# Kernel optimization log

Hardware: AMD Instinct MI355X
Metric: run time of the kernel (lower is better)

## Reference

```python
import jax, jax.numpy as jnp
import numpy as np

B, L, DW, DP = 128, 512, 256, 64
NF = 512          # num_filters == types == nr (forced by U.view / maxpool in source)
D = DW + 2 * DP   # 384
DWIN = 3 * D      # windowed feature width


def setup_inputs() -> dict:
    key = jax.random.key(0)
    ks = jax.random.split(key, 10)
    return {
        "x": jax.random.normal(ks[0], (B, L, DW), jnp.float32),
        "e1": jax.random.normal(ks[1], (B, DW), jnp.float32),
        "e2": jax.random.normal(ks[2], (B, DW), jnp.float32),
        "posVec": jax.random.normal(ks[3], (B, L, 2 * DP), jnp.float32),
        "We1": jax.random.normal(ks[4], (DW, DW), jnp.float32),
        "We2": jax.random.normal(ks[5], (DW, DW), jnp.float32),
        "U": jax.random.normal(ks[6], (NF, NF), jnp.float32),
        "conv_w": jax.random.normal(ks[7], (NF, DWIN), jnp.float32) * 0.02,
        "conv_b": jnp.zeros((NF,), jnp.float32),
        "rel_w": jax.random.normal(ks[8], (NF, NF), jnp.float32) * 0.02,  # y_embedding.weight (nr, num_filters)
    }


def reference(x, e1, e2, posVec, We1, We2, U, conv_w, conv_b, rel_w):
    # ---- input attention ----
    x_concat = jnp.concatenate([x, posVec], axis=-1)            # (B, L, D)
    px = jnp.pad(x_concat, ((0, 0), (1, 1), (0, 0)))            # pad seq by k=1
    w_concat = jnp.concatenate(
        [px[:, 0:L], px[:, 1:L + 1], px[:, 2:L + 2]], axis=-1)  # (B, L, 3D)
    A1 = jnp.einsum('bld,de,be->bl', x, We1, e1)                # (B, L)
    A2 = jnp.einsum('bld,de,be->bl', x, We2, e2)
    alpha = 0.5 * (jax.nn.softmax(A1, axis=1) + jax.nn.softmax(A2, axis=1))
    R = w_concat * alpha[:, :, None]                            # (B, L, 3D)
    # ---- convolution (kernel spans full window -> per-position linear) ----
    conv = jnp.tanh(jnp.einsum('bld,fd->bfl', R, conv_w) + conv_b[None, :, None])  # (B, F, L)
    # ---- attentive pooling ----
    G = jnp.einsum('bfl,ft,rt->blr', conv, U, rel_w)            # (B, L, nr)
    AP = jax.nn.softmax(G, axis=1)                              # softmax over seq positions
    wo = jnp.einsum('bfl,blr->bfr', conv, AP)                   # (B, F, nr)
    wo = jnp.max(wo, axis=2)                                    # MaxPool2d((1, types)) -> (B, F)
    wo = jax.nn.relu(wo)
    return wo, rel_w
```

## Files before the change

kernel.cpp:

```cpp
#include <hip/hip_runtime.h>
#include <hip/hip_bf16.h>

#define BB 128
#define LL 512
#define DW 256
#define DP 64
#define NF 512
#define DD 384
#define DWIN 1152
#define RR 512
#define LP 514

typedef __attribute__((ext_vector_type(8))) short short8;
typedef __attribute__((ext_vector_type(4))) short short4v;
typedef __attribute__((ext_vector_type(2))) short short2v;
typedef __attribute__((ext_vector_type(8))) _Float16 half8;
typedef __attribute__((ext_vector_type(4))) float f32x4;
typedef __attribute__((ext_vector_type(2))) float f32x2;

typedef __attribute__((address_space(1))) const void* gas_t;
typedef __attribute__((address_space(3))) void* las_t;

__device__ __forceinline__ void stage16(const void* g, void* l) {
    __builtin_amdgcn_global_load_lds((gas_t)g, (las_t)l, 16, 0, 0);
}

__device__ inline short f2h(float v) {
    _Float16 h = (_Float16)v;
    return *reinterpret_cast<short*>(&h);
}
__device__ inline int xcd_swz(int bid, int nwg) {
    return (bid & 7) * (nwg >> 3) + (bid >> 3);
}

__global__ void k_ve(const float* __restrict__ We1, const float* __restrict__ We2,
                     const float* __restrict__ e1, const float* __restrict__ e2,
                     float* __restrict__ v1, float* __restrict__ v2) {
    int b = blockIdx.x;
    int d = threadIdx.x;
    __shared__ float s1[DW], s2[DW];
    s1[d] = e1[b * DW + d];
    s2[d] = e2[b * DW + d];
    __syncthreads();
    float a1 = 0.f, a2 = 0.f;
    for (int e = 0; e < DW; ++e) {
        a1 += We1[d * DW + e] * s1[e];
        a2 += We2[d * DW + e] * s2[e];
    }
    v1[b * DW + d] = a1;
    v2[b * DW + d] = a2;
}

__global__ __launch_bounds__(256) void k_pack_logits(
    const float* __restrict__ x, const float* __restrict__ pv,
    const float* __restrict__ v1, const float* __restrict__ v2,
    short* __restrict__ pxp, float* __restrict__ A1, float* __restrict__ A2) {
    int gr = blockIdx.x * 4 + (threadIdx.x >> 6);
    int lane = threadIdx.x & 63;
    int b = gr / LP;
    int rr = gr - b * LP;
    short* dst = pxp + (size_t)gr * DD;
    if (rr == 0 || rr == LP - 1) {
        *(short4v*)(dst + lane * 4) = (short4v){0, 0, 0, 0};
        *(short2v*)(dst + 256 + lane * 2) = (short2v){0, 0};
        return;
    }
    int l = rr - 1;
    f32x4 xv = *(const f32x4*)(x + ((size_t)b * LL + l) * DW + lane * 4);
    f32x2 pvv = *(const f32x2*)(pv + ((size_t)b * LL + l) * (2 * DP) + lane * 2);
    f32x4 w1 = *(const f32x4*)(v1 + b * DW + lane * 4);
    f32x4 w2 = *(const f32x4*)(v2 + b * DW + lane * 4);
    float p1 = xv[0] * w1[0] + xv[1] * w1[1] + xv[2] * w1[2] + xv[3] * w1[3];
    float p2 = xv[0] * w2[0] + xv[1] * w2[1] + xv[2] * w2[2] + xv[3] * w2[3];
    for (int off = 32; off; off >>= 1) {
        p1 += __shfl_down(p1, off);
        p2 += __shfl_down(p2, off);
    }
    short4v ox;
#pragma unroll
    for (int j = 0; j < 4; ++j) ox[j] = f2h(xv[j]);
    *(short4v*)(dst + lane * 4) = ox;
    short2v op;
    op[0] = f2h(pvv[0]);
    op[1] = f2h(pvv[1]);
    *(short2v*)(dst + 256 + lane * 2) = op;
    if (lane == 0) { A1[b * LL + l] = p1; A2[b * LL + l] = p2; }
}

__global__ void k_alpha(const float* __restrict__ A1, const float* __restrict__ A2,
                        float* __restrict__ alpha) {
    int b = blockIdx.x;
    int l = threadIdx.x;
    __shared__ float s[LL];
    float a1 = A1[b * LL + l], a2 = A2[b * LL + l];

    s[l] = a1; __syncthreads();
    for (int st = 256; st; st >>= 1) { if (l < st) s[l] = fmaxf(s[l], s[l + st]); __syncthreads(); }
    float m1 = s[0]; __syncthreads();
    float e1x = expf(a1 - m1);
    s[l] = e1x; __syncthreads();
    for (int st = 256; st; st >>= 1) { if (l < st) s[l] += s[l + st]; __syncthreads(); }
    float d1 = s[0]; __syncthreads();

    s[l] = a2; __syncthreads();
    for (int st = 256; st; st >>= 1) { if (l < st) s[l] = fmaxf(s[l], s[l + st]); __syncthreads(); }
    float m2 = s[0]; __syncthreads();
    float e2x = expf(a2 - m2);
    s[l] = e2x; __syncthreads();
    for (int st = 256; st; st >>= 1) { if (l < st) s[l] += s[l + st]; __syncthreads(); }
    float d2 = s[0];

    alpha[b * LL + l] = 0.5f * (e1x / d1 + e2x / d2);
}

__global__ __launch_bounds__(256) void k_pack_w(const float* __restrict__ cw,
                                                short* __restrict__ cwb) {
    int idx = blockIdx.x * 256 + threadIdx.x;
    const float* src = cw + (size_t)idx * 8;
    f32x4 u0 = *(const f32x4*)(src);
    f32x4 u1 = *(const f32x4*)(src + 4);
    short8 v;
#pragma unroll
    for (int jj = 0; jj < 4; ++jj) { v[jj] = f2h(u0[jj]); v[jj + 4] = f2h(u1[jj]); }
    *(short8*)(cwb + (size_t)idx * 8) = v;
}

__global__ void k_w2t(const float* __restrict__ U, const float* __restrict__ relw,
                      short* __restrict__ Qf) {
    __shared__ float As[16][65], Bs[16][65];
    int r0 = blockIdx.y * 64, f0 = blockIdx.x * 64;
    int tid = threadIdx.x, ty = tid >> 4, tx = tid & 15;
    float acc[4][4] = {};
    for (int k0 = 0; k0 < NF; k0 += 16) {
        for (int i = 0; i < 4; ++i) {
            int lin = tid + 256 * i;
            int kk = lin & 15, mm = lin >> 4;
            As[kk][mm] = relw[(r0 + mm) * NF + k0 + kk];
            Bs[kk][mm] = U[(f0 + mm) * NF + k0 + kk];
        }
        __syncthreads();
        for (int kk = 0; kk < 16; ++kk) {
            float av[4], bv[4];
            for (int i = 0; i < 4; ++i) av[i] = As[kk][ty * 4 + i];
            for (int j = 0; j < 4; ++j) bv[j] = Bs[kk][tx * 4 + j];
            for (int i = 0; i < 4; ++i)
                for (int j = 0; j < 4; ++j) acc[i][j] += av[i] * bv[j];
        }
        __syncthreads();
    }
    for (int i = 0; i < 4; ++i)
        for (int j = 0; j < 4; ++j)
            Qf[(size_t)(r0 + ty * 4 + i) * NF + f0 + tx * 4 + j] = f2h(acc[i][j]);
}

__global__ __launch_bounds__(256) void k_conv_mfma(
    const short* __restrict__ pxp, const short* __restrict__ cwb,
    const float* __restrict__ conv_b, const float* __restrict__ alpha,
    short* __restrict__ conv_lf, short* __restrict__ conv_fl) {
    int wg = xcd_swz(blockIdx.x, 2048);
    int b = wg >> 4;
    int l0 = ((wg >> 2) & 3) * 128;
    int f0 = (wg & 3) * 128;
    int tid = threadIdx.x;
    int lane = tid & 63, w = tid >> 6;
    int wm = w >> 1, wn = w & 1;
    int lr = lane & 15, lg = lane >> 4;

    __shared__ __align__(16) char smem[34816];
    short (*As)[32] = (short(*)[32])smem;
    short (*Bs)[32] = (short(*)[32])(smem + 8192);
    short (*T)[136] = (short(*)[136])smem;

    f32x4 acc[4][4];
    for (int i = 0; i < 4; ++i)
        for (int j = 0; j < 4; ++j) acc[i][j] = (f32x4){0.f, 0.f, 0.f, 0.f};

    int rowA = lane >> 2;
    int sw = (lane & 3) ^ ((rowA >> 1) & 3);
    const short* gA = pxp + ((size_t)b * LP + l0 + w * 32 + rowA) * DD + sw * 8;
    const short* gB = cwb + (size_t)(f0 + w * 32 + rowA) * DWIN + sw * 8;
    short* lA = &As[w * 32][0];
    short* lB = &Bs[w * 32][0];
    int rsw = (lg ^ ((lr >> 1) & 3)) * 8;
    int rA = wm * 64, rB = wn * 64;

    for (int kb = 0; kb < 36; ++kb) {
        int k0 = kb * 32;
        stage16(gA + k0, lA);
        stage16(gA + 16 * DD + k0, lA + 16 * 32);
        stage16(gB + k0, lB);
        stage16(gB + (size_t)16 * DWIN + k0, lB + 16 * 32);
        __syncthreads();
        half8 af[4], bf[4];
#pragma unroll
        for (int mi = 0; mi < 4; ++mi)
            af[mi] = *(const half8*)(&As[rA + mi * 16 + lr][rsw]);
#pragma unroll
        for (int ni = 0; ni < 4; ++ni)
            bf[ni] = *(const half8*)(&Bs[rB + ni * 16 + lr][rsw]);
#pragma unroll
        for (int mi = 0; mi < 4; ++mi)
#pragma unroll
            for (int ni = 0; ni < 4; ++ni)
                acc[mi][ni] = __builtin_amdgcn_mfma_f32_16x16x32_f16(
                    af[mi], bf[ni], acc[mi][ni], 0, 0, 0);
        __syncthreads();
    }

    int lbase = l0 + wm * 64, fbase = f0 + wn * 64;
#pragma unroll
    for (int mi = 0; mi < 4; ++mi) {
        f32x4 av = *(const f32x4*)(alpha + (size_t)b * LL + lbase + mi * 16 + lg * 4);
        int lrow = lbase + mi * 16 + lg * 4;
#pragma unroll
        for (int ni = 0; ni < 4; ++ni) {
            int f = fbase + ni * 16 + lr;
            float bias = conv_b[f];
            short4v o;
#pragma unroll
            for (int r = 0; r < 4; ++r) {
                float val = tanhf(av[r] * acc[mi][ni][r] + bias);
                short sv = f2h(val);
                o[r] = sv;
                conv_lf[((size_t)b * LL + lrow + r) * NF + f] = sv;
            }
            *(short4v*)(&T[wn * 64 + ni * 16 + lr][wm * 64 + mi * 16 + lg * 4]) = o;
        }
    }
    __syncthreads();
#pragma unroll
    for (int i = 0; i < 8; ++i) {
        int lin = tid + 256 * i;
        int frow = lin >> 4;
        int q = lin & 15;
        short8 v = *(const short8*)(&T[frow][q * 8]);
        *(short8*)(conv_fl + ((size_t)b * NF + f0 + frow) * LL + l0 + q * 8) = v;
    }
}


__global__ __launch_bounds__(256) void k_g_mfma(
    const short* __restrict__ Qf,
    const short* __restrict__ convlf, _Float16* __restrict__ Gp) {
    int wg = xcd_swz(blockIdx.x, 2048);
    int b = wg >> 4;
    int r0 = ((wg >> 2) & 3) * 128;
    int l0 = (wg & 3) * 128;
    int tid = threadIdx.x, lane = tid & 63, w = tid >> 6;
    int wm = w >> 1, wn = w & 1;
    int lr = lane & 15, lg = lane >> 4;

    __shared__ __align__(16) short As[128][64];
    __shared__ __align__(16) short Bs[128][64];

    f32x4 acc[4][4];
    for (int i = 0; i < 4; ++i)
        for (int j = 0; j < 4; ++j) acc[i][j] = (f32x4){0.f, 0.f, 0.f, 0.f};

    int rowA = lane >> 3;
    int sw = (lane & 7) ^ rowA;
    const short* gA = Qf + (size_t)(r0 + w * 32 + rowA) * NF + sw * 8;
    const short* gB = convlf + (size_t)b * LL * NF + (size_t)(l0 + w * 32 + rowA) * NF + sw * 8;
    short* lA = &As[w * 32][0];
    short* lB = &Bs[w * 32][0];
    int rA = wm * 64, rB = wn * 64;
    int p7 = lr & 7;

    for (int kb = 0; kb < 8; ++kb) {
        int k0 = kb * 64;
#pragma unroll
        for (int c = 0; c < 4; ++c) {
            stage16(gA + (size_t)(8 * c) * NF + k0, lA + c * 8 * 64);
            stage16(gB + (size_t)(8 * c) * NF + k0, lB + c * 8 * 64);
        }
        __syncthreads();
#pragma unroll
        for (int kk = 0; kk < 2; ++kk) {
            half8 af[4], bf[4];
            int cs = ((kk << 2) + lg);
#pragma unroll
            for (int mi = 0; mi < 4; ++mi)
                af[mi] = *(const half8*)(&As[rA + mi * 16 + lr][(cs ^ p7) * 8]);
#pragma unroll
            for (int ni = 0; ni < 4; ++ni)
                bf[ni] = *(const half8*)(&Bs[rB + ni * 16 + lr][(cs ^ p7) * 8]);
#pragma unroll
            for (int mi = 0; mi < 4; ++mi)
#pragma unroll
                for (int ni = 0; ni < 4; ++ni)
                    acc[mi][ni] = __builtin_amdgcn_mfma_f32_16x16x32_f16(
                        af[mi], bf[ni], acc[mi][ni], 0, 0, 0);
        }
        __syncthreads();
    }

    int rbase = r0 + wm * 64, lbase = l0 + wn * 64;
#pragma unroll
    for (int mi = 0; mi < 4; ++mi)
#pragma unroll
        for (int ni = 0; ni < 4; ++ni)
#pragma unroll
            for (int rr = 0; rr < 4; ++rr) {
                int r = rbase + mi * 16 + lg * 4 + rr;
                int l = lbase + ni * 16 + lr;
                Gp[((size_t)b * RR + r) * LL + l] = (_Float16)acc[mi][ni][rr];
            }
}

__global__ __launch_bounds__(256) void k_softmax(_Float16* __restrict__ Gp) {
    const float LOG2E = 1.4426950408889634f;
    int row = blockIdx.x * 4 + (threadIdx.x >> 6);
    int lane = threadIdx.x & 63;
    _Float16* base = Gp + (size_t)row * LL;
    half8 hv = *(const half8*)(base + lane * 8);
    float v[8];
#pragma unroll
    for (int j = 0; j < 8; ++j) v[j] = (float)hv[j];
    float m = v[0];
#pragma unroll
    for (int j = 1; j < 8; ++j) m = fmaxf(m, v[j]);
    for (int off = 1; off < 64; off <<= 1) m = fmaxf(m, __shfl_xor(m, off));
    float s = 0.f;
    float p[8];
#pragma unroll
    for (int j = 0; j < 8; ++j) { p[j] = exp2f((v[j] - m) * LOG2E); s += p[j]; }
    for (int off = 1; off < 64; off <<= 1) s += __shfl_xor(s, off);
    float inv = 1.f / s;
    short8 o;
#pragma unroll
    for (int j = 0; j < 8; ++j) o[j] = f2h(p[j] * inv);
    *(short8*)((short*)base + lane * 8) = o;
}

__global__ __launch_bounds__(256) void k_wo_mfma(
    const short* __restrict__ convfl, const short* __restrict__ P,
    float* __restrict__ out) {
    int wg = xcd_swz(blockIdx.x, 2048);
    int b = wg >> 4;
    int f0 = ((wg >> 2) & 3) * 128;
    int r0 = (wg & 3) * 128;
    int tid = threadIdx.x, lane = tid & 63, w = tid >> 6;
    int wm = w >> 1, wn = w & 1;
    int lr = lane & 15, lg = lane >> 4;

    __shared__ __align__(16) short As[128][64];
    __shared__ __align__(16) short Bs[128][64];

    f32x4 acc[4][4];
    for (int i = 0; i < 4; ++i)
        for (int j = 0; j < 4; ++j) acc[i][j] = (f32x4){0.f, 0.f, 0.f, 0.f};

    int rowA = lane >> 3;
    int sw = (lane & 7) ^ rowA;
    const short* gA = convfl + (size_t)b * NF * LL + (size_t)(f0 + w * 32 + rowA) * LL + sw * 8;
    const short* gB = P + (size_t)b * RR * LL + (size_t)(r0 + w * 32 + rowA) * LL + sw * 8;
    short* lA = &As[w * 32][0];
    short* lB = &Bs[w * 32][0];
    int rA = wm * 64, rB = wn * 64;
    int p7 = lr & 7;

    for (int kb = 0; kb < 8; ++kb) {
        int k0 = kb * 64;
#pragma unroll
        for (int c = 0; c < 4; ++c) {
            stage16(gA + (size_t)(8 * c) * LL + k0, lA + c * 8 * 64);
            stage16(gB + (size_t)(8 * c) * LL + k0, lB + c * 8 * 64);
        }
        __syncthreads();
#pragma unroll
        for (int kk = 0; kk < 2; ++kk) {
            half8 af[4], bf[4];
            int cs = ((kk << 2) + lg);
#pragma unroll
            for (int mi = 0; mi < 4; ++mi)
                af[mi] = *(const half8*)(&As[rA + mi * 16 + lr][(cs ^ p7) * 8]);
#pragma unroll
            for (int ni = 0; ni < 4; ++ni)
                bf[ni] = *(const half8*)(&Bs[rB + ni * 16 + lr][(cs ^ p7) * 8]);
#pragma unroll
            for (int mi = 0; mi < 4; ++mi)
#pragma unroll
                for (int ni = 0; ni < 4; ++ni)
                    acc[mi][ni] = __builtin_amdgcn_mfma_f32_16x16x32_f16(
                        af[mi], bf[ni], acc[mi][ni], 0, 0, 0);
        }
        __syncthreads();
    }

    int fbase = f0 + wm * 64;
#pragma unroll
    for (int mi = 0; mi < 4; ++mi)
#pragma unroll
        for (int rr = 0; rr < 4; ++rr) {
            float m = acc[mi][0][rr];
#pragma unroll
            for (int ni = 1; ni < 4; ++ni) m = fmaxf(m, acc[mi][ni][rr]);
            m = fmaxf(m, __shfl_xor(m, 1));
            m = fmaxf(m, __shfl_xor(m, 2));
            m = fmaxf(m, __shfl_xor(m, 4));
            m = fmaxf(m, __shfl_xor(m, 8));
            if (lr == 0 && m > 0.f) {
                int f = fbase + mi * 16 + lg * 4 + rr;
                atomicMax((int*)&out[(size_t)b * NF + f], __float_as_int(m));
            }
        }
}

extern "C" void kernel_launch(void* const* d_in, const int* in_sizes, int n_in,
                              void* d_out, int out_size, void* d_ws, size_t ws_size,
                              hipStream_t stream) {
    const float* x      = (const float*)d_in[0];
    const float* e1     = (const float*)d_in[1];
    const float* e2     = (const float*)d_in[2];
    const float* posVec = (const float*)d_in[3];
    const float* We1    = (const float*)d_in[4];
    const float* We2    = (const float*)d_in[5];
    const float* U      = (const float*)d_in[6];
    const float* conv_w = (const float*)d_in[7];
    const float* conv_b = (const float*)d_in[8];
    const float* rel_w  = (const float*)d_in[9];
    float* out = (float*)d_out;

    char* p = (char*)d_ws;
    short* convlf = (short*)p;  p += (size_t)BB * LL * NF * 2;
    short* convfl = (short*)p;  p += (size_t)BB * NF * LL * 2;
    _Float16* Gp  = (_Float16*)p;  p += (size_t)BB * RR * LL * 2;
    short* pxp    = (short*)p;  p += (size_t)BB * LP * DD * 2;
    short* cwb    = (short*)p;  p += (size_t)NF * DWIN * 2;
    short* QfW    = (short*)p;  p += (size_t)RR * NF * 2;
    float* v1     = (float*)p;  p += (size_t)BB * DW * 4;
    float* v2     = (float*)p;  p += (size_t)BB * DW * 4;
    float* A1     = (float*)p;  p += (size_t)BB * LL * 4;
    float* A2     = (float*)p;  p += (size_t)BB * LL * 4;
    float* alpha  = (float*)p;  p += (size_t)BB * LL * 4;

    k_ve<<<BB, DW, 0, stream>>>(We1, We2, e1, e2, v1, v2);
    k_pack_logits<<<(BB * LP) / 4, 256, 0, stream>>>(x, posVec, v1, v2, pxp, A1, A2);
    k_alpha<<<BB, LL, 0, stream>>>(A1, A2, alpha);
    k_pack_w<<<(NF * DWIN / 8) / 256, 256, 0, stream>>>(conv_w, cwb);
    k_w2t<<<dim3(NF / 64, RR / 64), 256, 0, stream>>>(U, rel_w, QfW);
    k_conv_mfma<<<2048, 256, 0, stream>>>(pxp, cwb, conv_b, alpha, convlf, convfl);
    k_g_mfma<<<2048, 256, 0, stream>>>(QfW, convlf, Gp);
    k_softmax<<<(BB * RR) / 4, 256, 0, stream>>>(Gp);
    hipMemsetAsync(d_out, 0, (size_t)BB * NF * sizeof(float), stream);
    k_wo_mfma<<<2048, 256, 0, stream>>>(convfl, (const short*)Gp, out);
    hipMemcpyAsync(out + BB * NF, rel_w, (size_t)NF * RR * sizeof(float),
                   hipMemcpyDeviceToDevice, stream);
}
```

Measured before the change: 329.0 us.

## Fuse softmax over sequence into G GEMM epilogue with full-L tiles

Each G GEMM workgroup now covers the full sequence length (128 rows of r by all 512 positions, 512 threads, 8 waves). This lets the softmax over L run in the epilogue, using cross-lane shuffles and an LDS reduction across the four column waves. The separate softmax kernel and its extra read/write pass over the fp16 G buffer are removed. In exchange, the grid shrinks to 512 workgroups, each with 80KB of LDS and a much larger accumulator, so occupancy drops and fewer blocks are available to hide latency.

```diff
diff --git a/kernel.cpp b/kernel.cpp
--- a/kernel.cpp
+++ b/kernel.cpp
@@ -238,98 +238,140 @@
     }
 }
 
-
-__global__ __launch_bounds__(256) void k_g_mfma(
+__global__ __launch_bounds__(512) void k_g_mfma(
     const short* __restrict__ Qf,
     const short* __restrict__ convlf, _Float16* __restrict__ Gp) {
-    int wg = xcd_swz(blockIdx.x, 2048);
-    int b = wg >> 4;
-    int r0 = ((wg >> 2) & 3) * 128;
-    int l0 = (wg & 3) * 128;
+    const float LOG2E = 1.4426950408889634f;
+    int wg = xcd_swz(blockIdx.x, 512);
+    int b = wg >> 2;
+    int r0 = (wg & 3) * 128;
     int tid = threadIdx.x, lane = tid & 63, w = tid >> 6;
-    int wm = w >> 1, wn = w & 1;
+    int wm = w >> 2, wn = w & 3;
     int lr = lane & 15, lg = lane >> 4;
 
-    __shared__ __align__(16) short As[128][64];
-    __shared__ __align__(16) short Bs[128][64];
-
-    f32x4 acc[4][4];
+    __shared__ __align__(16) char smem[81920];
+    short* Ab = (short*)smem;
+    short* Bb = (short*)(smem + 16384);
+    float (*rowred)[4] = (float(*)[4])smem;
+
+    f32x4 acc[4][8];
+#pragma unroll
     for (int i = 0; i < 4; ++i)
-        for (int j = 0; j < 4; ++j) acc[i][j] = (f32x4){0.f, 0.f, 0.f, 0.f};
-
-    int rowA = lane >> 3;
-    int sw = (lane & 7) ^ rowA;
-    const short* gA = Qf + (size_t)(r0 + w * 32 + rowA) * NF + sw * 8;
-    const short* gB = convlf + (size_t)b * LL * NF + (size_t)(l0 + w * 32 + rowA) * NF + sw * 8;
-    short* lA = &As[w * 32][0];
-    short* lB = &Bs[w * 32][0];
-    int rA = wm * 64, rB = wn * 64;
+#pragma unroll
+        for (int j = 0; j < 8; ++j) acc[i][j] = (f32x4){0.f, 0.f, 0.f, 0.f};
+
+    int trow = tid >> 3;
+    int sw = (tid & 7) ^ (trow & 7);
+    const short* gA = Qf + (size_t)(r0 + trow) * NF + sw * 8;
+    const short* gB = convlf + (size_t)b * LL * NF + (size_t)trow * NF + sw * 8;
+    short* lAd = Ab + w * 512;
+    short* lBd = Bb + w * 512;
     int p7 = lr & 7;
 
     for (int kb = 0; kb < 8; ++kb) {
         int k0 = kb * 64;
 #pragma unroll
-        for (int c = 0; c < 4; ++c) {
-            stage16(gA + (size_t)(8 * c) * NF + k0, lA + c * 8 * 64);
-            stage16(gB + (size_t)(8 * c) * NF + k0, lB + c * 8 * 64);
-        }
+        for (int c = 0; c < 2; ++c)
+            stage16(gA + (size_t)(64 * c) * NF + k0, lAd + c * 4096);
+#pragma unroll
+        for (int c = 0; c < 8; ++c)
+            stage16(gB + (size_t)(64 * c) * NF + k0, lBd + c * 4096);
         __syncthreads();
 #pragma unroll
         for (int kk = 0; kk < 2; ++kk) {
-            half8 af[4], bf[4];
-            int cs = ((kk << 2) + lg);
+            int cs = (kk << 2) + lg;
+            half8 af[4], bf[8];
 #pragma unroll
             for (int mi = 0; mi < 4; ++mi)
-                af[mi] = *(const half8*)(&As[rA + mi * 16 + lr][(cs ^ p7) * 8]);
-#pragma unroll
-            for (int ni = 0; ni < 4; ++ni)
-                bf[ni] = *(const half8*)(&Bs[rB + ni * 16 + lr][(cs ^ p7) * 8]);
+                af[mi] = *(const half8*)(Ab + (wm * 64 + mi * 16 + lr) * 64 + ((cs ^ p7) * 8));
+#pragma unroll
+            for (int ni = 0; ni < 8; ++ni)
+                bf[ni] = *(const half8*)(Bb + (wn * 128 + ni * 16 + lr) * 64 + ((cs ^ p7) * 8));
 #pragma unroll
             for (int mi = 0; mi < 4; ++mi)
 #pragma unroll
-                for (int ni = 0; ni < 4; ++ni)
+                for (int ni = 0; ni < 8; ++ni)
                     acc[mi][ni] = __builtin_amdgcn_mfma_f32_16x16x32_f16(
                         af[mi], bf[ni], acc[mi][ni], 0, 0, 0);
         }
         __syncthreads();
     }
 
-    int rbase = r0 + wm * 64, lbase = l0 + wn * 64;
-#pragma unroll
-    for (int mi = 0; mi < 4; ++mi)
-#pragma unroll
-        for (int ni = 0; ni < 4; ++ni)
+    float mrow[4][4];
+#pragma unroll
+    for (int mi = 0; mi < 4; ++mi)
+#pragma unroll
+        for (int rr = 0; rr < 4; ++rr) {
+            float m = acc[mi][0][rr];
+#pragma unroll
+            for (int ni = 1; ni < 8; ++ni) m = fmaxf(m, acc[mi][ni][rr]);
+            m = fmaxf(m, __shfl_xor(m, 1));
+            m = fmaxf(m, __shfl_xor(m, 2));
+            m = fmaxf(m, __shfl_xor(m, 4));
+            m = fmaxf(m, __shfl_xor(m, 8));
+            mrow[mi][rr] = m;
+        }
+    if (lr == 0) {
+#pragma unroll
+        for (int mi = 0; mi < 4; ++mi)
+#pragma unroll
+            for (int rr = 0; rr < 4; ++rr)
+                rowred[wm * 64 + mi * 16 + lg * 4 + rr][wn] = mrow[mi][rr];
+    }
+    __syncthreads();
+#pragma unroll
+    for (int mi = 0; mi < 4; ++mi)
+#pragma unroll
+        for (int rr = 0; rr < 4; ++rr) {
+            f32x4 rv = *(const f32x4*)rowred[wm * 64 + mi * 16 + lg * 4 + rr];
+            mrow[mi][rr] = fmaxf(fmaxf(rv[0], rv[1]), fmaxf(rv[2], rv[3]));
+        }
+    __syncthreads();
+    float srow[4][4];
+#pragma unroll
+    for (int mi = 0; mi < 4; ++mi)
+#pragma unroll
+        for (int rr = 0; rr < 4; ++rr) {
+            float s = 0.f;
+            float m = mrow[mi][rr];
+#pragma unroll
+            for (int ni = 0; ni < 8; ++ni) {
+                float pp = exp2f((acc[mi][ni][rr] - m) * LOG2E);
+                acc[mi][ni][rr] = pp;
+                s += pp;
+            }
+            s += __shfl_xor(s, 1);
+            s += __shfl_xor(s, 2);
+            s += __shfl_xor(s, 4);
+            s += __shfl_xor(s, 8);
+            srow[mi][rr] = s;
+        }
+    if (lr == 0) {
+#pragma unroll
+        for (int mi = 0; mi < 4; ++mi)
+#pragma unroll
+            for (int rr = 0; rr < 4; ++rr)
+                rowred[wm * 64 + mi * 16 + lg * 4 + rr][wn] = srow[mi][rr];
+    }
+    __syncthreads();
+#pragma unroll
+    for (int mi = 0; mi < 4; ++mi)
+#pragma unroll
+        for (int rr = 0; rr < 4; ++rr) {
+            f32x4 rv = *(const f32x4*)rowred[wm * 64 + mi * 16 + lg * 4 + rr];
+            srow[mi][rr] = 1.f / (rv[0] + rv[1] + rv[2] + rv[3]);
+        }
+
+#pragma unroll
+    for (int mi = 0; mi < 4; ++mi)
+#pragma unroll
+        for (int ni = 0; ni < 8; ++ni)
 #pragma unroll
             for (int rr = 0; rr < 4; ++rr) {
-                int r = rbase + mi * 16 + lg * 4 + rr;
-                int l = lbase + ni * 16 + lr;
-                Gp[((size_t)b * RR + r) * LL + l] = (_Float16)acc[mi][ni][rr];
+                int r = r0 + wm * 64 + mi * 16 + lg * 4 + rr;
+                int l = wn * 128 + ni * 16 + lr;
+                Gp[((size_t)b * RR + r) * LL + l] = (_Float16)(acc[mi][ni][rr] * srow[mi][rr]);
             }
-}
-
-__global__ __launch_bounds__(256) void k_softmax(_Float16* __restrict__ Gp) {
-    const float LOG2E = 1.4426950408889634f;
-    int row = blockIdx.x * 4 + (threadIdx.x >> 6);
-    int lane = threadIdx.x & 63;
-    _Float16* base = Gp + (size_t)row * LL;
-    half8 hv = *(const half8*)(base + lane * 8);
-    float v[8];
-#pragma unroll
-    for (int j = 0; j < 8; ++j) v[j] = (float)hv[j];
-    float m = v[0];
-#pragma unroll
-    for (int j = 1; j < 8; ++j) m = fmaxf(m, v[j]);
-    for (int off = 1; off < 64; off <<= 1) m = fmaxf(m, __shfl_xor(m, off));
-    float s = 0.f;
-    float p[8];
-#pragma unroll
-    for (int j = 0; j < 8; ++j) { p[j] = exp2f((v[j] - m) * LOG2E); s += p[j]; }
-    for (int off = 1; off < 64; off <<= 1) s += __shfl_xor(s, off);
-    float inv = 1.f / s;
-    short8 o;
-#pragma unroll
-    for (int j = 0; j < 8; ++j) o[j] = f2h(p[j] * inv);
-    *(short8*)((short*)base + lane * 8) = o;
 }
 
 __global__ __launch_bounds__(256) void k_wo_mfma(
@@ -440,8 +482,7 @@
     k_pack_w<<<(NF * DWIN / 8) / 256, 256, 0, stream>>>(conv_w, cwb);
     k_w2t<<<dim3(NF / 64, RR / 64), 256, 0, stream>>>(U, rel_w, QfW);
     k_conv_mfma<<<2048, 256, 0, stream>>>(pxp, cwb, conv_b, alpha, convlf, convfl);
-    k_g_mfma<<<2048, 256, 0, stream>>>(QfW, convlf, Gp);
-    k_softmax<<<(BB * RR) / 4, 256, 0, stream>>>(Gp);
+    k_g_mfma<<<512, 512, 0, stream>>>(QfW, convlf, Gp);
     hipMemsetAsync(d_out, 0, (size_t)BB * NF * sizeof(float), stream);
     k_wo_mfma<<<2048, 256, 0, stream>>>(convfl, (const short*)Gp, out);
     hipMemcpyAsync(out + BB * NF, rel_w, (size_t)NF * RR * sizeof(float),
```

Measured after the change: 328.1 us. About the same (-0.3%).
